# Kernel optimization log

Measured on AMD Instinct MI355X. Metric: run time of the kernel, lower is better.

The kernel has to match this reference:

```python
import jax, jax.numpy as jnp
import numpy as np

N_NODES = 100000
N_EDGES = 1600000
D_IN = 128
D_OUT = 128


def setup_inputs() -> dict:
    key = jax.random.key(0)
    k1, k2, k3 = jax.random.split(key, 3)
    x = jax.random.normal(k1, (N_NODES, D_IN), dtype=jnp.float32)
    edge_index = jax.random.randint(k2, (2, N_EDGES), 0, N_NODES, dtype=jnp.int32)
    W = jax.random.normal(k3, (D_IN, D_OUT), dtype=jnp.float32) / np.sqrt(D_IN)
    b = jnp.zeros((D_OUT,), dtype=jnp.float32)
    return {"x": x, "edge_index": edge_index, "W": W, "b": b}


def reference(x, edge_index, W, b):
    """GCNConv (add self-loops, symmetric norm) + ReLU.
    out = relu(D^-1/2 (A+I) D^-1/2 X W + b)
    """
    N = x.shape[0]
    src, dst = edge_index[0], edge_index[1]
    loop = jnp.arange(N, dtype=src.dtype)
    src = jnp.concatenate([src, loop])  # [E+N]
    dst = jnp.concatenate([dst, loop])  # [E+N]

    # degree of target nodes (includes self-loop, so deg >= 1)
    deg = jax.ops.segment_sum(jnp.ones(dst.shape, dtype=x.dtype), dst,
                              num_segments=N)
    deg_inv_sqrt = jax.lax.rsqrt(deg)
    norm = deg_inv_sqrt[src] * deg_inv_sqrt[dst]  # [E+N]

    h = x @ W  # [N, D_OUT] — transform before aggregation (PyG GCNConv)
    msg = h[src] * norm[:, None]  # gather + normalize
    out = jax.ops.segment_sum(msg, dst, num_segments=N)  # scatter-add
    return jax.nn.relu(out + b)
```

## Files before the change

### kernel.cpp

```cpp
#include <hip/hip_runtime.h>

#define N_NODES 100000
#define N_EDGES 1600000
#define D 128
#define SUBW 32
#define NSUB2 3125
#define NC 196
#define BSH 9
#define BMSK 511
#define CAPC 12288
#define CAP3 9728
#define CAPS2 1024
#define CHUNK3 4096
#define BIND_BLOCKS ((N_EDGES + CHUNK3 - 1) / CHUNK3)
#define GEMM2_BLOCKS ((N_NODES + 127) / 128)
#define STAGE_MAX (CHUNK3 + NC * 16)
#define NGRP (STAGE_MAX / 16)
#define CCSTRIDE 16

typedef __attribute__((ext_vector_type(8))) short short8;
typedef __attribute__((ext_vector_type(4))) float float4v;

__device__ inline unsigned short f2bf(float f) {
    unsigned u = __float_as_uint(f);
    unsigned r = (u + 0x7fffu + ((u >> 16) & 1u)) >> 16;
    return (unsigned short)r;
}
__device__ inline float bflo(unsigned int p) { return __uint_as_float(p << 16); }
__device__ inline float bfhi(unsigned int p) { return __uint_as_float(p & 0xffff0000u); }

__global__ void probe_convert_kernel(const unsigned int* __restrict__ xw,
                                     const void* __restrict__ b,
                                     const void* __restrict__ Wv,
                                     int* __restrict__ flag, float* __restrict__ bfv,
                                     unsigned short* __restrict__ Wbf,
                                     int* __restrict__ ccnt) {
    __shared__ int cnt;
    if (threadIdx.x == 0) cnt = 0;
    __syncthreads();
    unsigned low = xw[threadIdx.x] & 0xFFFFu;
    unsigned e = (low >> 7) & 0xFFu;
    atomicAdd(&cnt, (int)((e == 0u) || (e >= 107u && e <= 147u)));
    __syncthreads();
    int m = (cnt >= 192);
    if (threadIdx.x == 0) *flag = m;
    if (threadIdx.x < D)
        bfv[threadIdx.x] = m ? bflo(((const unsigned short*)b)[threadIdx.x])
                             : ((const float*)b)[threadIdx.x];
    for (int i = threadIdx.x; i < D * D; i += 256)
        Wbf[i] = m ? ((const unsigned short*)Wv)[i] : f2bf(((const float*)Wv)[i]);
    for (int i = threadIdx.x; i < NC * CCSTRIDE; i += 256) ccnt[i] = 0;
}

__global__ void __launch_bounds__(256) binD_kernel(
        const int* __restrict__ src, const int* __restrict__ dst,
        int* __restrict__ ccnt, unsigned* __restrict__ recg) {
    __shared__ __align__(16) unsigned stg[STAGE_MAX];
    __shared__ int cnt[NC], cpad[NC], ofs[NC], base[NC], place[NC];
    __shared__ unsigned short g2b[NGRP];
    __shared__ int tot;

    int tid = threadIdx.x;
    int e0 = blockIdx.x * CHUNK3;
    int e1 = e0 + CHUNK3 < N_EDGES ? e0 + CHUNK3 : N_EDGES;
    if (tid < NC) cnt[tid] = 0;
    __syncthreads();

    unsigned recs[16];
    int bks[16];
    #pragma unroll
    for (int k = 0; k < 4; ++k) {
        int i = e0 + tid * 4 + k * 1024;
        if (i + 3 < e1) {
            int4 d4 = *(const int4*)&dst[i];
            int4 s4 = *(const int4*)&src[i];
            recs[k * 4 + 0] = (unsigned)s4.x | ((unsigned)(d4.x & BMSK) << 17); bks[k * 4 + 0] = d4.x >> BSH;
            recs[k * 4 + 1] = (unsigned)s4.y | ((unsigned)(d4.y & BMSK) << 17); bks[k * 4 + 1] = d4.y >> BSH;
            recs[k * 4 + 2] = (unsigned)s4.z | ((unsigned)(d4.z & BMSK) << 17); bks[k * 4 + 2] = d4.z >> BSH;
            recs[k * 4 + 3] = (unsigned)s4.w | ((unsigned)(d4.w & BMSK) << 17); bks[k * 4 + 3] = d4.w >> BSH;
        } else {
            bks[k * 4 + 0] = -1; bks[k * 4 + 1] = -1; bks[k * 4 + 2] = -1; bks[k * 4 + 3] = -1;
            recs[k * 4 + 0] = 0; recs[k * 4 + 1] = 0; recs[k * 4 + 2] = 0; recs[k * 4 + 3] = 0;
        }
    }
    #pragma unroll
    for (int k = 0; k < 16; ++k)
        if (bks[k] >= 0) atomicAdd(&cnt[bks[k]], 1);
    __syncthreads();

    if (tid < NC) {
        int c = cnt[tid];
        int p = (c + 15) & ~15;
        cpad[tid] = p;
        base[tid] = p ? atomicAdd(&ccnt[tid * CCSTRIDE], p) : 0;
    }
    __syncthreads();
    if (tid == 0) {
        int s = 0;
        for (int k = 0; k < NC; ++k) { ofs[k] = s; place[k] = s; s += cpad[k]; }
        tot = s;
    }
    __syncthreads();
    if (tid < NC) {
        int o = ofs[tid], e = o + cpad[tid];
        for (int j = o + cnt[tid]; j < e; ++j) stg[j] = 0xFFFFFFFFu;
        for (int g = o >> 4; g < (e >> 4); ++g) g2b[g] = (unsigned short)tid;
    }
    __syncthreads();

    #pragma unroll
    for (int k = 0; k < 16; ++k)
        if (bks[k] >= 0) {
            int p = atomicAdd(&place[bks[k]], 1);
            stg[p] = recs[k];
        }
    __syncthreads();

    int tot_ = tot;
    for (int j = tid * 4; j < tot_; j += 1024) {
        int lo = g2b[j >> 4];
        int gi = base[lo] + (j - ofs[lo]);
        if (gi < CAPC)
            *(uint4*)&recg[(size_t)lo * CAPC + gi] = *(const uint4*)&stg[j];
    }
}

__global__ void __launch_bounds__(512) fused_sortgemm_kernel(
        unsigned* __restrict__ recg, const int* __restrict__ ccnt,
        int* __restrict__ deg, int* __restrict__ nodeofs, float* __restrict__ dis,
        const void* __restrict__ xv, const unsigned short* __restrict__ Wbf,
        const int* __restrict__ flag, unsigned short* __restrict__ h) {
    __shared__ union {
        struct {
            int hist[512], ofs[512], place[512], wsum[8];
            __align__(16) unsigned s_srt[CAP3];
        } s;
        unsigned short Wt[D * 136];
    } u;

    int tid = threadIdx.x;

    if (blockIdx.x < NC) {
        int b = blockIdx.x;
        u.s.hist[tid] = 0;
        __syncthreads();
        int count = ccnt[b * CCSTRIDE]; if (count > CAPC) count = CAPC;
        const unsigned* r = recg + (size_t)b * CAPC;
        for (int i = tid * 4; i + 3 < count; i += 2048) {
            uint4 w4 = *(const uint4*)&r[i];
            if (w4.x != 0xFFFFFFFFu) atomicAdd(&u.s.hist[w4.x >> 17], 1);
            if (w4.y != 0xFFFFFFFFu) atomicAdd(&u.s.hist[w4.y >> 17], 1);
            if (w4.z != 0xFFFFFFFFu) atomicAdd(&u.s.hist[w4.z >> 17], 1);
            if (w4.w != 0xFFFFFFFFu) atomicAdd(&u.s.hist[w4.w >> 17], 1);
        }
        __syncthreads();

        int lane = tid & 63, wave = tid >> 6;
        int h0 = u.s.hist[tid];
        int v = h0;
        #pragma unroll
        for (int dsh = 1; dsh < 64; dsh <<= 1) {
            int uu = __shfl_up(v, dsh);
            if (lane >= dsh) v += uu;
        }
        if (lane == 63) u.s.wsum[wave] = v;
        __syncthreads();
        int wbase = 0;
        #pragma unroll
        for (int k = 0; k < 8; ++k) if (k < wave) wbase += u.s.wsum[k];
        int e0v = wbase + v - h0;
        u.s.ofs[tid] = e0v; u.s.place[tid] = e0v;
        int n = b * 512 + tid;
        deg[n] = h0;
        nodeofs[n] = e0v;
        dis[n] = rsqrtf((float)(h0 + 1));
        __syncthreads();

        for (int i = tid * 4; i + 3 < count; i += 2048) {
            uint4 w4 = *(const uint4*)&r[i];
            if (w4.x != 0xFFFFFFFFu) { int p = atomicAdd(&u.s.place[w4.x >> 17], 1); if (p < CAP3) u.s.s_srt[p] = w4.x & 0x1FFFFu; }
            if (w4.y != 0xFFFFFFFFu) { int p = atomicAdd(&u.s.place[w4.y >> 17], 1); if (p < CAP3) u.s.s_srt[p] = w4.y & 0x1FFFFu; }
            if (w4.z != 0xFFFFFFFFu) { int p = atomicAdd(&u.s.place[w4.z >> 17], 1); if (p < CAP3) u.s.s_srt[p] = w4.z & 0x1FFFFu; }
            if (w4.w != 0xFFFFFFFFu) { int p = atomicAdd(&u.s.place[w4.w >> 17], 1); if (p < CAP3) u.s.s_srt[p] = w4.w & 0x1FFFFu; }
        }
        __syncthreads();

        int total = u.s.ofs[511] + u.s.hist[511];
        int totR = (total + 15) & ~15; if (totR > CAP3) totR = CAP3;
        unsigned* w = recg + (size_t)b * CAPC;
        for (int j = tid * 4; j < totR; j += 2048)
            *(uint4*)&w[j] = *(const uint4*)&u.s.s_srt[j];
    } else {
        int bid2 = blockIdx.x - NC;
        int m = *flag;
        for (int idx = tid; idx < D * D; idx += 512) {
            int k = idx >> 7, c = idx & 127;
            u.Wt[c * 136 + k] = Wbf[idx];
        }
        __syncthreads();

        int wave = tid >> 6, lane = tid & 63;
        int row0 = (bid2 * 8 + wave) * 16;
        if (row0 >= N_NODES) return;
        int r = lane & 15, quad = lane >> 4;

        short8 a[4];
        if (m) {
            const unsigned short* xr = (const unsigned short*)xv + (size_t)(row0 + r) * D + quad * 8;
            #pragma unroll
            for (int t = 0; t < 4; ++t) a[t] = *(const short8*)(xr + t * 32);
        } else {
            const float* xr = (const float*)xv + (size_t)(row0 + r) * D + quad * 8;
            #pragma unroll
            for (int t = 0; t < 4; ++t) {
                float4 f0 = *(const float4*)(xr + t * 32);
                float4 f1 = *(const float4*)(xr + t * 32 + 4);
                a[t][0] = (short)f2bf(f0.x); a[t][1] = (short)f2bf(f0.y);
                a[t][2] = (short)f2bf(f0.z); a[t][3] = (short)f2bf(f0.w);
                a[t][4] = (short)f2bf(f1.x); a[t][5] = (short)f2bf(f1.y);
                a[t][6] = (short)f2bf(f1.z); a[t][7] = (short)f2bf(f1.w);
            }
        }

        #pragma unroll
        for (int ct = 0; ct < 8; ++ct) {
            int col0 = ct * 16;
            float4v c = {0.f, 0.f, 0.f, 0.f};
            #pragma unroll
            for (int t = 0; t < 4; ++t) {
                short8 bfr = *(const short8*)&u.Wt[(col0 + r) * 136 + t * 32 + quad * 8];
                c = __builtin_amdgcn_mfma_f32_16x16x32_bf16(a[t], bfr, c, 0, 0, 0);
            }
            #pragma unroll
            for (int reg = 0; reg < 4; ++reg) {
                int orow = row0 + quad * 4 + reg;
                h[(size_t)orow * D + col0 + r] = f2bf(c[reg]);
            }
        }
    }
}

__global__ void __launch_bounds__(256) agg5_kernel(
        const unsigned* __restrict__ srt2, const int* __restrict__ nodeofs,
        const int* __restrict__ deg, const float* __restrict__ dis,
        const float* __restrict__ bfv, const int* __restrict__ flag,
        const unsigned short* __restrict__ h, void* __restrict__ out) {
    __shared__ unsigned srt[CAPS2];
    __shared__ int l_ofs[SUBW];
    __shared__ int l_deg[SUBW];
    __shared__ float lbias[D];

    int sub = blockIdx.x, tid = threadIdx.x;
    int n0 = sub * SUBW;
    int B = n0 >> BSH, loc0 = n0 & BMSK;
    if (tid < SUBW) {
        l_ofs[tid] = nodeofs[B * 512 + loc0 + tid];
        l_deg[tid] = deg[n0 + tid];
    }
    if (tid < D) lbias[tid] = bfv[tid];
    __syncthreads();

    int base0 = l_ofs[0];
    int span = (l_ofs[SUBW - 1] + l_deg[SUBW - 1]) - base0;
    if (span > CAPS2) span = CAPS2;
    if (span > CAP3 - base0) span = CAP3 - base0;
    const unsigned* sb = srt2 + (size_t)B * CAPC + base0;
    for (int i = tid; i < span; i += 256) srt[i] = sb[i];
    __syncthreads();

    const uint4* h4 = (const uint4*)h;
    int wave = tid >> 6, lane = tid & 63;
    int q = lane >> 4, c16 = lane & 15;
    int m = *flag;

    for (int t = 0; t < 8; ++t) {
        int nl = wave * 8 + t;
        int n = n0 + nl;
        int o = l_ofs[nl] - base0;
        int cnt = l_deg[nl];
        int e_end = o + cnt; if (e_end > span) e_end = span;

        uint4 sp = make_uint4(0u, 0u, 0u, 0u);
        if (q == 0) sp = h4[(size_t)n * 16 + c16];

        float acc[8] = {0.f, 0.f, 0.f, 0.f, 0.f, 0.f, 0.f, 0.f};
        int j = o + q;
        for (; j + 4 < e_end; j += 8) {
            unsigned s0 = srt[j];
            unsigned s1 = srt[j + 4];
            uint4 p0 = h4[(size_t)s0 * 16 + c16];
            uint4 p1 = h4[(size_t)s1 * 16 + c16];
            float w0 = dis[s0], w1 = dis[s1];
            acc[0] += w0 * bflo(p0.x); acc[1] += w0 * bfhi(p0.x);
            acc[2] += w0 * bflo(p0.y); acc[3] += w0 * bfhi(p0.y);
            acc[4] += w0 * bflo(p0.z); acc[5] += w0 * bfhi(p0.z);
            acc[6] += w0 * bflo(p0.w); acc[7] += w0 * bfhi(p0.w);
            acc[0] += w1 * bflo(p1.x); acc[1] += w1 * bfhi(p1.x);
            acc[2] += w1 * bflo(p1.y); acc[3] += w1 * bfhi(p1.y);
            acc[4] += w1 * bflo(p1.z); acc[5] += w1 * bfhi(p1.z);
            acc[6] += w1 * bflo(p1.w); acc[7] += w1 * bfhi(p1.w);
        }
        if (j < e_end) {
            unsigned s0 = srt[j];
            uint4 p0 = h4[(size_t)s0 * 16 + c16];
            float w0 = dis[s0];
            acc[0] += w0 * bflo(p0.x); acc[1] += w0 * bfhi(p0.x);
            acc[2] += w0 * bflo(p0.y); acc[3] += w0 * bfhi(p0.y);
            acc[4] += w0 * bflo(p0.z); acc[5] += w0 * bfhi(p0.z);
            acc[6] += w0 * bflo(p0.w); acc[7] += w0 * bfhi(p0.w);
        }
        #pragma unroll
        for (int i = 0; i < 8; ++i) {
            acc[i] += __shfl_xor(acc[i], 16);
            acc[i] += __shfl_xor(acc[i], 32);
        }

        if (q == 0) {
            float dn = rsqrtf((float)(cnt + 1));
            float v[8];
            v[0] = fmaxf(dn * (acc[0] + dn * bflo(sp.x)) + lbias[c16 * 8 + 0], 0.f);
            v[1] = fmaxf(dn * (acc[1] + dn * bfhi(sp.x)) + lbias[c16 * 8 + 1], 0.f);
            v[2] = fmaxf(dn * (acc[2] + dn * bflo(sp.y)) + lbias[c16 * 8 + 2], 0.f);
            v[3] = fmaxf(dn * (acc[3] + dn * bfhi(sp.y)) + lbias[c16 * 8 + 3], 0.f);
            v[4] = fmaxf(dn * (acc[4] + dn * bflo(sp.z)) + lbias[c16 * 8 + 4], 0.f);
            v[5] = fmaxf(dn * (acc[5] + dn * bfhi(sp.z)) + lbias[c16 * 8 + 5], 0.f);
            v[6] = fmaxf(dn * (acc[6] + dn * bflo(sp.w)) + lbias[c16 * 8 + 6], 0.f);
            v[7] = fmaxf(dn * (acc[7] + dn * bfhi(sp.w)) + lbias[c16 * 8 + 7], 0.f);
            if (m) {
                uint4 pk;
                pk.x = ((unsigned)f2bf(v[1]) << 16) | f2bf(v[0]);
                pk.y = ((unsigned)f2bf(v[3]) << 16) | f2bf(v[2]);
                pk.z = ((unsigned)f2bf(v[5]) << 16) | f2bf(v[4]);
                pk.w = ((unsigned)f2bf(v[7]) << 16) | f2bf(v[6]);
                ((uint4*)out)[(size_t)n * 16 + c16] = pk;
            } else {
                float4 f0 = make_float4(v[0], v[1], v[2], v[3]);
                float4 f1 = make_float4(v[4], v[5], v[6], v[7]);
                float4* of = (float4*)((float*)out + (size_t)n * D + c16 * 8);
                of[0] = f0; of[1] = f1;
            }
        }
    }
}

extern "C" void kernel_launch(void* const* d_in, const int* in_sizes, int n_in,
                              void* d_out, int out_size, void* d_ws, size_t ws_size,
                              hipStream_t stream) {
    const void* x = nullptr; const int* ei = nullptr;
    const void* W = nullptr; const void* b = nullptr;
    for (int i = 0; i < n_in; ++i) {
        if      (in_sizes[i] == N_NODES * D) x  = d_in[i];
        else if (in_sizes[i] == 2 * N_EDGES) ei = (const int*)d_in[i];
        else if (in_sizes[i] == D * D)       W  = d_in[i];
        else if (in_sizes[i] == D)           b  = d_in[i];
    }
    if (!x || !ei || !W || !b) {
        x = d_in[0]; ei = (const int*)d_in[1]; W = d_in[2]; b = d_in[3];
    }
    const int* src = ei;
    const int* dst = ei + N_EDGES;

    char* ws = (char*)d_ws;
    int*      flag    = (int*)ws;
    int*      ccnt    = (int*)(ws + 16);
    float*    bfv     = (float*)(ccnt + NC * CCSTRIDE);
    unsigned short* Wbf = (unsigned short*)(bfv + D);
    int*      deg     = (int*)(Wbf + D * D);
    int*      nodeofs = deg + NC * 512;
    float*    dis     = (float*)(nodeofs + NC * 512);
    unsigned* recg    = (unsigned*)(dis + NC * 512);
    unsigned short* h = (unsigned short*)(recg + (size_t)NC * CAPC);

    probe_convert_kernel<<<1, 256, 0, stream>>>((const unsigned int*)x, b, W,
                                                flag, bfv, Wbf, ccnt);

    binD_kernel<<<BIND_BLOCKS, 256, 0, stream>>>(src, dst, ccnt, recg);

    fused_sortgemm_kernel<<<NC + GEMM2_BLOCKS, 512, 0, stream>>>(
        recg, ccnt, deg, nodeofs, dis, x, Wbf, flag, h);

    agg5_kernel<<<NSUB2, 256, 0, stream>>>(recg, nodeofs, deg, dis, bfv, flag, h, d_out);
}
```

Baseline: 242.9 us.

## Split fused sort/GEMM kernel, widen binning blocks, transpose MFMA output stores, split agg launch

The fused sort+GEMM kernel is split back into separate gemm and sortdeg kernels, which removes the shared-memory union and lets each kernel size its LDS independently. The binning kernel moves to 512 threads with 8 records per thread. The GEMM swaps the MFMA operands so each lane holds four consecutive columns of one row and writes them as a packed uint2, replacing scattered 2-byte stores. The aggregation is issued as two half launches with a sub-block offset. Together these add kernel launches and give up the overlap of sort blocks with GEMM blocks, in exchange for simpler kernels and better-coalesced stores.

```diff
diff --git a/kernel.cpp b/kernel.cpp
--- a/kernel.cpp
+++ b/kernel.cpp
@@ -5,6 +5,7 @@
 #define D 128
 #define SUBW 32
 #define NSUB2 3125
+#define AGG_HALF 1563
 #define NC 196
 #define BSH 9
 #define BMSK 511
@@ -13,7 +14,7 @@
 #define CAPS2 1024
 #define CHUNK3 4096
 #define BIND_BLOCKS ((N_EDGES + CHUNK3 - 1) / CHUNK3)
-#define GEMM2_BLOCKS ((N_NODES + 127) / 128)
+#define GEMM_BLOCKS ((N_NODES + 127) / 128)
 #define STAGE_MAX (CHUNK3 + NC * 16)
 #define NGRP (STAGE_MAX / 16)
 #define CCSTRIDE 16
@@ -52,7 +53,7 @@
     for (int i = threadIdx.x; i < NC * CCSTRIDE; i += 256) ccnt[i] = 0;
 }
 
-__global__ void __launch_bounds__(256) binD_kernel(
+__global__ void __launch_bounds__(512) binD_kernel(
         const int* __restrict__ src, const int* __restrict__ dst,
         int* __restrict__ ccnt, unsigned* __restrict__ recg) {
     __shared__ __align__(16) unsigned stg[STAGE_MAX];
@@ -66,11 +67,11 @@
     if (tid < NC) cnt[tid] = 0;
     __syncthreads();
 
-    unsigned recs[16];
-    int bks[16];
-    #pragma unroll
-    for (int k = 0; k < 4; ++k) {
-        int i = e0 + tid * 4 + k * 1024;
+    unsigned recs[8];
+    int bks[8];
+    #pragma unroll
+    for (int k = 0; k < 2; ++k) {
+        int i = e0 + tid * 4 + k * 2048;
         if (i + 3 < e1) {
             int4 d4 = *(const int4*)&dst[i];
             int4 s4 = *(const int4*)&src[i];
@@ -84,7 +85,7 @@
         }
     }
     #pragma unroll
-    for (int k = 0; k < 16; ++k)
+    for (int k = 0; k < 8; ++k)
         if (bks[k] >= 0) atomicAdd(&cnt[bks[k]], 1);
     __syncthreads();
 
@@ -109,7 +110,7 @@
     __syncthreads();
 
     #pragma unroll
-    for (int k = 0; k < 16; ++k)
+    for (int k = 0; k < 8; ++k)
         if (bks[k] >= 0) {
             int p = atomicAdd(&place[bks[k]], 1);
             stg[p] = recs[k];
@@ -117,7 +118,7 @@
     __syncthreads();
 
     int tot_ = tot;
-    for (int j = tid * 4; j < tot_; j += 1024) {
+    for (int j = tid * 4; j < tot_; j += 2048) {
         int lo = g2b[j >> 4];
         int gi = base[lo] + (j - ofs[lo]);
         if (gi < CAPC)
@@ -125,132 +126,127 @@
     }
 }
 
-__global__ void __launch_bounds__(512) fused_sortgemm_kernel(
-        unsigned* __restrict__ recg, const int* __restrict__ ccnt,
-        int* __restrict__ deg, int* __restrict__ nodeofs, float* __restrict__ dis,
+__global__ void __launch_bounds__(512) gemm_kernel(
         const void* __restrict__ xv, const unsigned short* __restrict__ Wbf,
         const int* __restrict__ flag, unsigned short* __restrict__ h) {
-    __shared__ union {
-        struct {
-            int hist[512], ofs[512], place[512], wsum[8];
-            __align__(16) unsigned s_srt[CAP3];
-        } s;
-        unsigned short Wt[D * 136];
-    } u;
-
+    __shared__ unsigned short Wt[D * 136];
     int tid = threadIdx.x;
-
-    if (blockIdx.x < NC) {
-        int b = blockIdx.x;
-        u.s.hist[tid] = 0;
-        __syncthreads();
-        int count = ccnt[b * CCSTRIDE]; if (count > CAPC) count = CAPC;
-        const unsigned* r = recg + (size_t)b * CAPC;
-        for (int i = tid * 4; i + 3 < count; i += 2048) {
-            uint4 w4 = *(const uint4*)&r[i];
-            if (w4.x != 0xFFFFFFFFu) atomicAdd(&u.s.hist[w4.x >> 17], 1);
-            if (w4.y != 0xFFFFFFFFu) atomicAdd(&u.s.hist[w4.y >> 17], 1);
-            if (w4.z != 0xFFFFFFFFu) atomicAdd(&u.s.hist[w4.z >> 17], 1);
-            if (w4.w != 0xFFFFFFFFu) atomicAdd(&u.s.hist[w4.w >> 17], 1);
-        }
-        __syncthreads();
-
-        int lane = tid & 63, wave = tid >> 6;
-        int h0 = u.s.hist[tid];
-        int v = h0;
+    int m = *flag;
+    for (int idx = tid; idx < D * D; idx += 512) {
+        int k = idx >> 7, c = idx & 127;
+        Wt[c * 136 + k] = Wbf[idx];
+    }
+    __syncthreads();
+
+    int wave = tid >> 6, lane = tid & 63;
+    int row0 = (int)blockIdx.x * 128 + wave * 16;
+    if (row0 >= N_NODES) return;
+    int r = lane & 15, quad = lane >> 4;
+
+    short8 a[4];
+    if (m) {
+        const unsigned short* xr = (const unsigned short*)xv + (size_t)(row0 + r) * D + quad * 8;
         #pragma unroll
-        for (int dsh = 1; dsh < 64; dsh <<= 1) {
-            int uu = __shfl_up(v, dsh);
-            if (lane >= dsh) v += uu;
-        }
-        if (lane == 63) u.s.wsum[wave] = v;
-        __syncthreads();
-        int wbase = 0;
+        for (int t = 0; t < 4; ++t) a[t] = *(const short8*)(xr + t * 32);
+    } else {
+        const float* xr = (const float*)xv + (size_t)(row0 + r) * D + quad * 8;
         #pragma unroll
-        for (int k = 0; k < 8; ++k) if (k < wave) wbase += u.s.wsum[k];
-        int e0v = wbase + v - h0;
-        u.s.ofs[tid] = e0v; u.s.place[tid] = e0v;
-        int n = b * 512 + tid;
-        deg[n] = h0;
-        nodeofs[n] = e0v;
-        dis[n] = rsqrtf((float)(h0 + 1));
-        __syncthreads();
-
-        for (int i = tid * 4; i + 3 < count; i += 2048) {
-            uint4 w4 = *(const uint4*)&r[i];
-            if (w4.x != 0xFFFFFFFFu) { int p = atomicAdd(&u.s.place[w4.x >> 17], 1); if (p < CAP3) u.s.s_srt[p] = w4.x & 0x1FFFFu; }
-            if (w4.y != 0xFFFFFFFFu) { int p = atomicAdd(&u.s.place[w4.y >> 17], 1); if (p < CAP3) u.s.s_srt[p] = w4.y & 0x1FFFFu; }
-            if (w4.z != 0xFFFFFFFFu) { int p = atomicAdd(&u.s.place[w4.z >> 17], 1); if (p < CAP3) u.s.s_srt[p] = w4.z & 0x1FFFFu; }
-            if (w4.w != 0xFFFFFFFFu) { int p = atomicAdd(&u.s.place[w4.w >> 17], 1); if (p < CAP3) u.s.s_srt[p] = w4.w & 0x1FFFFu; }
-        }
-        __syncthreads();
-
-        int total = u.s.ofs[511] + u.s.hist[511];
-        int totR = (total + 15) & ~15; if (totR > CAP3) totR = CAP3;
-        unsigned* w = recg + (size_t)b * CAPC;
-        for (int j = tid * 4; j < totR; j += 2048)
-            *(uint4*)&w[j] = *(const uint4*)&u.s.s_srt[j];
-    } else {
-        int bid2 = blockIdx.x - NC;
-        int m = *flag;
-        for (int idx = tid; idx < D * D; idx += 512) {
-            int k = idx >> 7, c = idx & 127;
-            u.Wt[c * 136 + k] = Wbf[idx];
-        }
-        __syncthreads();
-
-        int wave = tid >> 6, lane = tid & 63;
-        int row0 = (bid2 * 8 + wave) * 16;
-        if (row0 >= N_NODES) return;
-        int r = lane & 15, quad = lane >> 4;
-
-        short8 a[4];
-        if (m) {
-            const unsigned short* xr = (const unsigned short*)xv + (size_t)(row0 + r) * D + quad * 8;
-            #pragma unroll
-            for (int t = 0; t < 4; ++t) a[t] = *(const short8*)(xr + t * 32);
-        } else {
-            const float* xr = (const float*)xv + (size_t)(row0 + r) * D + quad * 8;
-            #pragma unroll
-            for (int t = 0; t < 4; ++t) {
-                float4 f0 = *(const float4*)(xr + t * 32);
-                float4 f1 = *(const float4*)(xr + t * 32 + 4);
-                a[t][0] = (short)f2bf(f0.x); a[t][1] = (short)f2bf(f0.y);
-                a[t][2] = (short)f2bf(f0.z); a[t][3] = (short)f2bf(f0.w);
-                a[t][4] = (short)f2bf(f1.x); a[t][5] = (short)f2bf(f1.y);
-                a[t][6] = (short)f2bf(f1.z); a[t][7] = (short)f2bf(f1.w);
-            }
-        }
-
+        for (int t = 0; t < 4; ++t) {
+            float4 f0 = *(const float4*)(xr + t * 32);
+            float4 f1 = *(const float4*)(xr + t * 32 + 4);
+            a[t][0] = (short)f2bf(f0.x); a[t][1] = (short)f2bf(f0.y);
+            a[t][2] = (short)f2bf(f0.z); a[t][3] = (short)f2bf(f0.w);
+            a[t][4] = (short)f2bf(f1.x); a[t][5] = (short)f2bf(f1.y);
+            a[t][6] = (short)f2bf(f1.z); a[t][7] = (short)f2bf(f1.w);
+        }
+    }
+
+    #pragma unroll
+    for (int ct = 0; ct < 8; ++ct) {
+        int col0 = ct * 16;
+        float4v c4 = {0.f, 0.f, 0.f, 0.f};
         #pragma unroll
-        for (int ct = 0; ct < 8; ++ct) {
-            int col0 = ct * 16;
-            float4v c = {0.f, 0.f, 0.f, 0.f};
-            #pragma unroll
-            for (int t = 0; t < 4; ++t) {
-                short8 bfr = *(const short8*)&u.Wt[(col0 + r) * 136 + t * 32 + quad * 8];
-                c = __builtin_amdgcn_mfma_f32_16x16x32_bf16(a[t], bfr, c, 0, 0, 0);
-            }
-            #pragma unroll
-            for (int reg = 0; reg < 4; ++reg) {
-                int orow = row0 + quad * 4 + reg;
-                h[(size_t)orow * D + col0 + r] = f2bf(c[reg]);
-            }
-        }
-    }
+        for (int t = 0; t < 4; ++t) {
+            short8 bfr = *(const short8*)&Wt[(col0 + r) * 136 + t * 32 + quad * 8];
+            c4 = __builtin_amdgcn_mfma_f32_16x16x32_bf16(bfr, a[t], c4, 0, 0, 0);
+        }
+        unsigned u0 = (unsigned)f2bf(c4[0]) | ((unsigned)f2bf(c4[1]) << 16);
+        unsigned u1 = (unsigned)f2bf(c4[2]) | ((unsigned)f2bf(c4[3]) << 16);
+        *(uint2*)&h[(size_t)(row0 + r) * D + col0 + quad * 4] = make_uint2(u0, u1);
+    }
+}
+
+__global__ void __launch_bounds__(512) sortdeg_kernel(
+        unsigned* __restrict__ recg, const int* __restrict__ ccnt,
+        int* __restrict__ deg, int* __restrict__ nodeofs, float* __restrict__ dis) {
+    __shared__ int hist[512];
+    __shared__ int ofs[512];
+    __shared__ int place[512];
+    __shared__ int wsum[8];
+    __shared__ __align__(16) unsigned s_srt[CAP3];
+
+    int b = blockIdx.x, tid = threadIdx.x;
+    hist[tid] = 0;
+    __syncthreads();
+    int count = ccnt[b * CCSTRIDE]; if (count > CAPC) count = CAPC;
+    const unsigned* r = recg + (size_t)b * CAPC;
+    for (int i = tid * 4; i + 3 < count; i += 2048) {
+        uint4 w4 = *(const uint4*)&r[i];
+        if (w4.x != 0xFFFFFFFFu) atomicAdd(&hist[w4.x >> 17], 1);
+        if (w4.y != 0xFFFFFFFFu) atomicAdd(&hist[w4.y >> 17], 1);
+        if (w4.z != 0xFFFFFFFFu) atomicAdd(&hist[w4.z >> 17], 1);
+        if (w4.w != 0xFFFFFFFFu) atomicAdd(&hist[w4.w >> 17], 1);
+    }
+    __syncthreads();
+
+    int lane = tid & 63, wave = tid >> 6;
+    int h0 = hist[tid];
+    int v = h0;
+    #pragma unroll
+    for (int dsh = 1; dsh < 64; dsh <<= 1) {
+        int uu = __shfl_up(v, dsh);
+        if (lane >= dsh) v += uu;
+    }
+    if (lane == 63) wsum[wave] = v;
+    __syncthreads();
+    int wbase = 0;
+    #pragma unroll
+    for (int k = 0; k < 8; ++k) if (k < wave) wbase += wsum[k];
+    int e0v = wbase + v - h0;
+    ofs[tid] = e0v; place[tid] = e0v;
+    int n = b * 512 + tid;
+    deg[n] = h0;
+    nodeofs[n] = e0v;
+    dis[n] = rsqrtf((float)(h0 + 1));
+    __syncthreads();
+
+    for (int i = tid * 4; i + 3 < count; i += 2048) {
+        uint4 w4 = *(const uint4*)&r[i];
+        if (w4.x != 0xFFFFFFFFu) { int p = atomicAdd(&place[w4.x >> 17], 1); if (p < CAP3) s_srt[p] = w4.x & 0x1FFFFu; }
+        if (w4.y != 0xFFFFFFFFu) { int p = atomicAdd(&place[w4.y >> 17], 1); if (p < CAP3) s_srt[p] = w4.y & 0x1FFFFu; }
+        if (w4.z != 0xFFFFFFFFu) { int p = atomicAdd(&place[w4.z >> 17], 1); if (p < CAP3) s_srt[p] = w4.z & 0x1FFFFu; }
+        if (w4.w != 0xFFFFFFFFu) { int p = atomicAdd(&place[w4.w >> 17], 1); if (p < CAP3) s_srt[p] = w4.w & 0x1FFFFu; }
+    }
+    __syncthreads();
+
+    int total = ofs[511] + hist[511];
+    int totR = (total + 15) & ~15; if (totR > CAP3) totR = CAP3;
+    unsigned* w = recg + (size_t)b * CAPC;
+    for (int j = tid * 4; j < totR; j += 2048)
+        *(uint4*)&w[j] = *(const uint4*)&s_srt[j];
 }
 
 __global__ void __launch_bounds__(256) agg5_kernel(
         const unsigned* __restrict__ srt2, const int* __restrict__ nodeofs,
         const int* __restrict__ deg, const float* __restrict__ dis,
         const float* __restrict__ bfv, const int* __restrict__ flag,
-        const unsigned short* __restrict__ h, void* __restrict__ out) {
+        const unsigned short* __restrict__ h, void* __restrict__ out, int sub0) {
     __shared__ unsigned srt[CAPS2];
     __shared__ int l_ofs[SUBW];
     __shared__ int l_deg[SUBW];
     __shared__ float lbias[D];
 
-    int sub = blockIdx.x, tid = threadIdx.x;
+    int sub = blockIdx.x + sub0, tid = threadIdx.x;
     int n0 = sub * SUBW;
     int B = n0 >> BSH, loc0 = n0 & BMSK;
     if (tid < SUBW) {
@@ -374,10 +370,14 @@
     probe_convert_kernel<<<1, 256, 0, stream>>>((const unsigned int*)x, b, W,
                                                 flag, bfv, Wbf, ccnt);
 
-    binD_kernel<<<BIND_BLOCKS, 256, 0, stream>>>(src, dst, ccnt, recg);
-
-    fused_sortgemm_kernel<<<NC + GEMM2_BLOCKS, 512, 0, stream>>>(
-        recg, ccnt, deg, nodeofs, dis, x, Wbf, flag, h);
-
-    agg5_kernel<<<NSUB2, 256, 0, stream>>>(recg, nodeofs, deg, dis, bfv, flag, h, d_out);
-}
+    binD_kernel<<<BIND_BLOCKS, 512, 0, stream>>>(src, dst, ccnt, recg);
+
+    gemm_kernel<<<GEMM_BLOCKS, 512, 0, stream>>>(x, Wbf, flag, h);
+
+    sortdeg_kernel<<<NC, 512, 0, stream>>>(recg, ccnt, deg, nodeofs, dis);
+
+    agg5_kernel<<<AGG_HALF, 256, 0, stream>>>(recg, nodeofs, deg, dis, bfv, flag, h,
+                                              d_out, 0);
+    agg5_kernel<<<NSUB2 - AGG_HALF, 256, 0, stream>>>(recg, nodeofs, deg, dis, bfv,
+                                                      flag, h, d_out, AGG_HALF);
+}
```

After: 260.2 us. +7.1%, slower.
